# Optimization experiments

Hardware: AMD Instinct MI355X
Metric: run time of the kernel (lower is better)

## Reference

```python
import jax, jax.numpy as jnp
import numpy as np

HEADS = 6
WS = 16          # window_size
OWS = 24         # overlap_win_size
DIM = 192
TABLE = (WS + OWS - 1) ** 2  # 1521


def setup_inputs() -> dict:
    key = jax.random.key(0)
    k1, k2, k3, k4, k5, k6 = jax.random.split(key, 6)
    b = 256
    nq = WS * WS          # 256
    n = OWS * OWS         # 576
    x_q = jax.random.normal(k1, (b, nq, DIM), dtype=jnp.float32)
    x_kv = jax.random.normal(k2, (b, n, DIM), dtype=jnp.float32)
    rpi = jax.random.randint(k3, (nq, n), 0, TABLE, dtype=jnp.int64)
    Wq = jax.random.normal(k4, (DIM, DIM), dtype=jnp.float32) * 0.02
    Wkv = jax.random.normal(k5, (2 * DIM, DIM), dtype=jnp.float32) * 0.02
    bias_table = jax.random.normal(k6, (TABLE, HEADS), dtype=jnp.float32) * 0.02
    return {"x_q": x_q, "x_kv": x_kv, "rpi": rpi, "Wq": Wq, "Wkv": Wkv, "bias_table": bias_table}


def reference(x_q, x_kv, rpi, Wq, Wkv, bias_table):
    b, nq, dim = x_q.shape
    n = x_kv.shape[1]
    hd = dim // HEADS
    scale = hd ** (-0.5)

    # projections (torch Linear: y = x @ W^T)
    q = (x_q @ Wq.T).reshape(b, nq, HEADS, hd).transpose(0, 2, 1, 3)      # b h nq d
    kv = x_kv @ Wkv.T                                                    # b n 2*dim
    k, v = jnp.split(kv, 2, axis=-1)
    k = k.reshape(b, n, HEADS, hd).transpose(0, 2, 1, 3)                  # b h n d
    v = v.reshape(b, n, HEADS, hd).transpose(0, 2, 1, 3)                  # b h n d

    attn = scale * jnp.einsum('bhqd,bhkd->bhqk', q, k)                    # b h nq n

    # gathered relative-position bias: table[rpi] -> (nq, n, h)
    rpb = bias_table[rpi.reshape(-1)].reshape(nq, n, HEADS)
    # nq < n branch in source: permute(2, 0, 1) -> (h, nq, n)
    rpb = rpb.transpose(2, 0, 1)

    attn = jax.nn.softmax(attn + rpb[None], axis=-1)
    out = jnp.einsum('bhqk,bhkd->bhqd', attn, v)                          # b h nq d
    out = out.transpose(0, 2, 1, 3).reshape(b, nq, dim)
    return out
```

## Files before the change

### kernel.cpp

```cpp
#include <hip/hip_runtime.h>
#include <cstdint>

typedef unsigned short u16;
typedef short s16x8 __attribute__((ext_vector_type(8)));
typedef float f32x4 __attribute__((ext_vector_type(4)));
typedef float f32x16 __attribute__((ext_vector_type(16)));

#if __has_builtin(__builtin_amdgcn_exp2f)
#define EXP2(x) __builtin_amdgcn_exp2f(x)
#else
#define EXP2(x) __expf((x)*0.6931471805599453f)
#endif

__device__ __forceinline__ u16 f2bf(float x) {
  uint32_t u = __builtin_bit_cast(uint32_t, x);
  u += 0x7FFFu + ((u >> 16) & 1u);
  return (u16)(u >> 16);
}
__device__ __forceinline__ float bf2f(u16 v) {
  return __builtin_bit_cast(float, (uint32_t)v << 16);
}
__device__ __forceinline__ uint32_t pk_bf16(float lo, float hi) {
  uint32_t ul = __builtin_bit_cast(uint32_t, lo);
  uint32_t uh = __builtin_bit_cast(uint32_t, hi);
  ul += 0x7FFFu + ((ul >> 16) & 1u);
  uh += 0x7FFFu + ((uh >> 16) & 1u);
  return __builtin_amdgcn_perm(uh, ul, 0x07060302u);
}
__device__ __forceinline__ f32x4 mfma16(s16x8 a, s16x8 b, f32x4 c) {
  return __builtin_amdgcn_mfma_f32_16x16x32_bf16(a, b, c, 0, 0, 0);
}
__device__ __forceinline__ f32x16 mfma32(s16x8 a, s16x8 b, f32x16 c) {
  return __builtin_amdgcn_mfma_f32_32x32x16_bf16(a, b, c, 0, 0, 0);
}
__device__ __forceinline__ s16x8 ld_frag(const u16* p) {
  uint4 v = *(const uint4*)p;
  return __builtin_bit_cast(s16x8, v);
}

__global__ void prep_w(const float* __restrict__ Wq, const float* __restrict__ Wkv,
                       u16* __restrict__ wqs, u16* __restrict__ wkvs) {
  int tid = blockIdx.x * 256 + threadIdx.x;
  if (tid >= 13824) return;
  bool isQ = tid < 4608;
  int id = isQ ? tid : tid - 4608;
  int lane = id & 63, fk = id >> 6;
  int kk = fk % 6, fb = fk / 6;
  int f = fb * 16 + (lane & 15), k0 = kk * 32 + ((lane >> 4) << 3);
  const float* src = (isQ ? Wq : Wkv) + (size_t)f * 192 + k0;
  const float sc = isQ ? 0.2550348583f : 1.0f;
  float4 a = ((const float4*)src)[0], b = ((const float4*)src)[1];
  uint4 o;
  o.x = pk_bf16(a.x * sc, a.y * sc); o.y = pk_bf16(a.z * sc, a.w * sc);
  o.z = pk_bf16(b.x * sc, b.y * sc); o.w = pk_bf16(b.z * sc, b.w * sc);
  *(uint4*)&(isQ ? wqs : wkvs)[(size_t)id * 8] = o;
}

__global__ void build_rpb(const int* __restrict__ rpi, const float* __restrict__ table,
                          u16* __restrict__ rpb) {
  const int bi = blockIdx.x;
  const int wv = bi & 7, hk = bi >> 3;
  const int h = hk / 18, kt = hk - h * 18;
  const int lane = threadIdx.x;
  const int u = lane >> 5, l31 = lane & 31;
  const int q = (wv << 5) + l31;
  const int n0 = (kt << 5) + (u << 2);
  u16 vals[16];
#pragma unroll
  for (int g = 0; g < 4; ++g) {
    int4 id4 = *(const int4*)&rpi[q * 576 + n0 + (g << 3)];
    vals[(g << 2) + 0] = f2bf(table[id4.x * 6 + h] * 1.4426950409f);
    vals[(g << 2) + 1] = f2bf(table[id4.y * 6 + h] * 1.4426950409f);
    vals[(g << 2) + 2] = f2bf(table[id4.z * 6 + h] * 1.4426950409f);
    vals[(g << 2) + 3] = f2bf(table[id4.w * 6 + h] * 1.4426950409f);
  }
  uint4* dst = (uint4*)&rpb[((size_t)hk * 512 + (wv << 6) + lane) * 16];
  dst[0] = *(uint4*)&vals[0];
  dst[1] = *(uint4*)&vals[8];
}

template <int G, int MODE>
__device__ __forceinline__ void proj_body(const float* __restrict__ A,
                                          const u16* __restrict__ W,
                                          u16* __restrict__ outQ, u16* __restrict__ outK,
                                          u16* __restrict__ outV, int blk0,
                                          u16* __restrict__ lds) {
  const int t = threadIdx.x, lane = t & 63, w = t >> 6, c = lane & 15, hi = lane >> 4;
  s16x8 wf[G][6];
#pragma unroll
  for (int f = 0; f < G; ++f)
#pragma unroll
    for (int kk = 0; kk < 6; ++kk)
      wf[f][kk] = ld_frag(&W[((size_t)(((w * G + f) * 6 + kk) * 64 + lane)) * 8]);
  const int srow = t >> 4, scol = (t & 15) * 12;
  float4 r0, r1, r2;
  auto ISSUE = [&](int i) {
    const float* src = A + (size_t)((blk0 * 8 + i) * 16 + srow) * 192 + scol;
    r0 = ((const float4*)src)[0];
    r1 = ((const float4*)src)[1];
    r2 = ((const float4*)src)[2];
  };
  auto WRITE = [&](int slot) {
    u16* sl = lds + slot * 3072;
#pragma unroll
    for (int j = 0; j < 3; ++j) {
      float4 v = (j == 0) ? r0 : (j == 1) ? r1 : r2;
      const int c0 = scol + j * 4, kk = c0 >> 5, rem = c0 & 31;
      const int h2 = rem >> 3, e0 = rem & 7;
      uint2 pv;
      pv.x = pk_bf16(v.x, v.y);
      pv.y = pk_bf16(v.z, v.w);
      *(uint2*)&sl[((kk << 6) + (h2 << 4) + srow) * 8 + e0] = pv;
    }
  };
  ISSUE(0); WRITE(0);
  ISSUE(1);
  for (int i = 0; i < 8; ++i) {
    __syncthreads();
    if (i + 1 < 8) WRITE((i + 1) % 3);
    if (i + 2 < 8) ISSUE(i + 2);
    const u16* sl = lds + (i % 3) * 3072;
    s16x8 af[6];
#pragma unroll
    for (int kk = 0; kk < 6; ++kk)
      af[kk] = ld_frag(&sl[((kk << 6) + lane) << 3]);
    f32x4 acc[G];
#pragma unroll
    for (int f = 0; f < G; ++f) acc[f] = f32x4{0.f, 0.f, 0.f, 0.f};
#pragma unroll
    for (int kk = 0; kk < 6; ++kk)
#pragma unroll
      for (int f = 0; f < G; ++f)
        acc[f] = mfma16(wf[f][kk], af[kk], acc[f]);
    const int m = (blk0 * 8 + i) * 16 + c;
#pragma unroll
    for (int f = 0; f < G; ++f) {
      const int fb = ((w * G + f) << 4) + (hi << 2);
      uint2 pv;
      pv.x = pk_bf16(acc[f][0], acc[f][1]);
      pv.y = pk_bf16(acc[f][2], acc[f][3]);
      if (MODE == 0) {
        int b = m >> 8, q = m & 255, hh = fb >> 5, d = fb & 31;
        *(uint2*)&outQ[((((size_t)(b * 6 + hh)) << 8) + q) * 32 + d] = pv;
      } else {
        int b = m / 576, tok = m - b * 576;
        if (fb >= 192) {
          int f2 = fb - 192, hh = f2 >> 5, d = f2 & 31;
          *(uint2*)&outV[(((size_t)(b * 6 + hh)) * 576 + tok) * 32 + d] = pv;
        } else {
          int hh = fb >> 5, dd = fb & 31;
          int half = dd >> 4, uu = (dd >> 3) & 1, e0 = dd & 7;
          int ktt = tok >> 5, lt = tok & 31;
          *(uint2*)&outK[(size_t)((b * 6 + hh) * 18 + ktt) * 1024 +
                         half * 512 + uu * 256 + lt * 8 + e0] = pv;
        }
      }
    }
  }
}

__launch_bounds__(256, 2)
__global__ void proj_all(const float* __restrict__ xq, const float* __restrict__ xkv,
                         const u16* __restrict__ wqs, const u16* __restrict__ wkvs,
                         u16* __restrict__ Qws, u16* __restrict__ Kws,
                         u16* __restrict__ Vws) {
  __shared__ __align__(16) u16 lds[9216];
  int blk = blockIdx.x;
  if (blk < 512) proj_body<3, 0>(xq, wqs, Qws, nullptr, nullptr, blk, lds);
  else           proj_body<6, 1>(xkv, wkvs, nullptr, Kws, Vws, blk - 512, lds);
}

#define VSTR 600
__launch_bounds__(512)
__global__ void attn(const u16* __restrict__ Qws, const u16* __restrict__ Kws,
                     const u16* __restrict__ Vws, const u16* __restrict__ rpb,
                     float* __restrict__ out) {
  __shared__ __align__(16) u16 Vt[32 * VSTR];
  const int bh = blockIdx.x, b = bh / 6, h = bh - b * 6;
  const size_t kvbase = (size_t)bh * 576 * 32;
  const int t = threadIdx.x;
  for (int key = t; key < 576; key += 512) {
    int kk = key & 31, k15 = kk & 15;
    int p = ((kk >> 4) << 4) | (((k15 >> 2) & 1) << 3) | ((k15 >> 3) << 2) | (k15 & 3);
    int col = ((key >> 5) << 5) + p;
    const uint4* src = (const uint4*)&Vws[kvbase + (size_t)key * 32];
    uint4 r[4] = {src[0], src[1], src[2], src[3]};
    const u16* vs = (const u16*)r;
#pragma unroll
    for (int d = 0; d < 32; ++d) Vt[d * VSTR + col] = vs[d];
  }
  const int lane = t & 63, l31 = lane & 31, u = lane >> 5, w = t >> 6;
  const int qg = (w << 5) + l31;
  s16x8 qf[2];
#pragma unroll
  for (int m = 0; m < 2; ++m)
    qf[m] = ld_frag(&Qws[((size_t)bh * 256 + qg) * 32 + (m << 4) + (u << 3)]);
  __syncthreads();
  f32x16 oacc;
#pragma unroll
  for (int r = 0; r < 16; ++r) oacc[r] = 0.f;
  float psum = 0.f;
  const u16* kfb = Kws + (size_t)bh * 18432 + (size_t)lane * 8;
  const u16* bp0 = rpb + (size_t)h * 147456 + (size_t)t * 16;
  s16x8 kA[2], kB[2];
  uint4 bA[2], bB[2];
  kA[0] = ld_frag(kfb);        kB[0] = ld_frag(kfb + 512);
  kA[1] = ld_frag(kfb + 1024); kB[1] = ld_frag(kfb + 1536);
  bA[0] = *(const uint4*)(bp0);        bB[0] = *(const uint4*)(bp0 + 8);
  bA[1] = *(const uint4*)(bp0 + 8192); bB[1] = *(const uint4*)(bp0 + 8192 + 8);
#pragma unroll 2
  for (int kt = 0; kt < 18; ++kt) {
    const int k0 = kt << 5, cur = kt & 1;
    s16x8 vf0 = ld_frag(&Vt[l31 * VSTR + k0 + (u << 3)]);
    s16x8 vf1 = ld_frag(&Vt[l31 * VSTR + k0 + 16 + (u << 3)]);
    f32x16 st;
#pragma unroll
    for (int r = 0; r < 16; ++r) st[r] = 0.f;
    st = mfma32(kA[cur], qf[0], st);
    st = mfma32(kB[cur], qf[1], st);
    uint4 bAc = bA[cur], bBc = bB[cur];
    if (kt < 16) {
      kA[cur] = ld_frag(kfb + (size_t)(kt + 2) * 1024);
      kB[cur] = ld_frag(kfb + (size_t)(kt + 2) * 1024 + 512);
      bA[cur] = *(const uint4*)(bp0 + (size_t)(kt + 2) * 8192);
      bB[cur] = *(const uint4*)(bp0 + (size_t)(kt + 2) * 8192 + 8);
    }
    const u16* b0 = (const u16*)&bAc;
    const u16* b1 = (const u16*)&bBc;
    float e[16];
#pragma unroll
    for (int r = 0; r < 8; ++r)
      e[r] = EXP2(st[r] + bf2f(b0[r]));
#pragma unroll
    for (int r = 8; r < 16; ++r)
      e[r] = EXP2(st[r] + bf2f(b1[r - 8]));
    psum += (((e[0] + e[1]) + (e[2] + e[3])) + ((e[4] + e[5]) + (e[6] + e[7]))) +
            (((e[8] + e[9]) + (e[10] + e[11])) + ((e[12] + e[13]) + (e[14] + e[15])));
    uint4 pa, pb;
    pa.x = pk_bf16(e[0], e[1]);   pa.y = pk_bf16(e[2], e[3]);
    pa.z = pk_bf16(e[4], e[5]);   pa.w = pk_bf16(e[6], e[7]);
    pb.x = pk_bf16(e[8], e[9]);   pb.y = pk_bf16(e[10], e[11]);
    pb.z = pk_bf16(e[12], e[13]); pb.w = pk_bf16(e[14], e[15]);
    s16x8 pf0 = __builtin_bit_cast(s16x8, pa);
    s16x8 pf1 = __builtin_bit_cast(s16x8, pb);
    oacc = mfma32(vf0, pf0, oacc);
    oacc = mfma32(vf1, pf1, oacc);
  }
  float tot = psum + __shfl_xor(psum, 32);
  float rs = 1.0f / tot;
  float* op = out + ((size_t)b * 256 + qg) * 192 + h * 32 + (u << 2);
#pragma unroll
  for (int g = 0; g < 4; ++g) {
    float4 o;
    o.x = oacc[(g << 2) + 0] * rs; o.y = oacc[(g << 2) + 1] * rs;
    o.z = oacc[(g << 2) + 2] * rs; o.w = oacc[(g << 2) + 3] * rs;
    *(float4*)(op + (g << 3)) = o;
  }
}

extern "C" void kernel_launch(void* const* d_in, const int* in_sizes, int n_in,
                              void* d_out, int out_size, void* d_ws, size_t ws_size,
                              hipStream_t stream) {
  const float* x_q   = (const float*)d_in[0];
  const float* x_kv  = (const float*)d_in[1];
  const int*   rpi   = (const int*)d_in[2];
  const float* Wq    = (const float*)d_in[3];
  const float* Wkv   = (const float*)d_in[4];
  const float* table = (const float*)d_in[5];
  float* out = (float*)d_out;

  char* ws = (char*)d_ws;
  u16* wqs  = (u16*)(ws);
  u16* wkvs = (u16*)(ws + 73728);
  u16* rpb  = (u16*)(ws + 221184);
  u16* Qws  = (u16*)(ws + 1990656);
  u16* Kws  = (u16*)(ws + 27156480);
  u16* Vws  = (u16*)(ws + 83779584);

  prep_w<<<54, 256, 0, stream>>>(Wq, Wkv, wqs, wkvs);
  build_rpb<<<864, 64, 0, stream>>>(rpi, table, rpb);
  proj_all<<<1664, 256, 0, stream>>>(x_q, x_kv, wqs, wkvs, Qws, Kws, Vws);
  attn<<<1536, 512, 0, stream>>>(Qws, Kws, Vws, rpb, out);
}
```

Baseline: 337.2 us.

## Load full 128-row tile into LDS upfront instead of triple-buffered pipeline

The projection kernel now has each thread load half a row (24 float4s) of the block's 128-row input tile at once. It converts the values to bf16 into a padded LDS layout (stride 17) to avoid bank conflicts, then runs all 8 MFMA sub-tiles after a single barrier. This removes the per-iteration barriers and the small three-slot software pipeline and issues more memory loads in flight per thread. The cost is more LDS per block (about 52 KB) and many live registers, which may lower occupancy, and no compute now overlaps the loads.

```diff
diff --git a/kernel.cpp b/kernel.cpp
--- a/kernel.cpp
+++ b/kernel.cpp
@@ -79,51 +79,53 @@
   dst[1] = *(uint4*)&vals[8];
 }
 
+#define TPW 17
+#define TILE_U16 (24 * TPW * 8)
 template <int G, int MODE>
 __device__ __forceinline__ void proj_body(const float* __restrict__ A,
                                           const u16* __restrict__ W,
                                           u16* __restrict__ outQ, u16* __restrict__ outK,
-                                          u16* __restrict__ outV, int blk0,
+                                          u16* __restrict__ outV, int blk,
                                           u16* __restrict__ lds) {
   const int t = threadIdx.x, lane = t & 63, w = t >> 6, c = lane & 15, hi = lane >> 4;
+  const int row0 = blk << 7;
+  {
+    const int row = t >> 1, halfc = (t & 1) * 96;
+    const float* src = A + (size_t)(row0 + row) * 192 + halfc;
+    u16* dst = lds + (row >> 4) * TILE_U16;
+    const int srow = row & 15;
+    float4 v[24];
+#pragma unroll
+    for (int j = 0; j < 24; ++j) v[j] = ((const float4*)src)[j];
+#pragma unroll
+    for (int j = 0; j < 24; ++j) {
+      const int c0 = halfc + (j << 2);
+      const int kk = c0 >> 5, h2 = (c0 >> 3) & 3, e0 = c0 & 7;
+      uint2 pv;
+      pv.x = pk_bf16(v[j].x, v[j].y);
+      pv.y = pk_bf16(v[j].z, v[j].w);
+      *(uint2*)&dst[(((kk << 2) + h2) * TPW + srow) * 8 + e0] = pv;
+    }
+  }
   s16x8 wf[G][6];
 #pragma unroll
   for (int f = 0; f < G; ++f)
 #pragma unroll
     for (int kk = 0; kk < 6; ++kk)
       wf[f][kk] = ld_frag(&W[((size_t)(((w * G + f) * 6 + kk) * 64 + lane)) * 8]);
-  const int srow = t >> 4, scol = (t & 15) * 12;
-  float4 r0, r1, r2;
-  auto ISSUE = [&](int i) {
-    const float* src = A + (size_t)((blk0 * 8 + i) * 16 + srow) * 192 + scol;
-    r0 = ((const float4*)src)[0];
-    r1 = ((const float4*)src)[1];
-    r2 = ((const float4*)src)[2];
-  };
-  auto WRITE = [&](int slot) {
-    u16* sl = lds + slot * 3072;
-#pragma unroll
-    for (int j = 0; j < 3; ++j) {
-      float4 v = (j == 0) ? r0 : (j == 1) ? r1 : r2;
-      const int c0 = scol + j * 4, kk = c0 >> 5, rem = c0 & 31;
-      const int h2 = rem >> 3, e0 = rem & 7;
-      uint2 pv;
-      pv.x = pk_bf16(v.x, v.y);
-      pv.y = pk_bf16(v.z, v.w);
-      *(uint2*)&sl[((kk << 6) + (h2 << 4) + srow) * 8 + e0] = pv;
-    }
-  };
-  ISSUE(0); WRITE(0);
-  ISSUE(1);
+#pragma unroll
+  for (int f = 0; f < G; ++f)
+#pragma unroll
+    for (int kk = 0; kk < 6; ++kk)
+      asm volatile("" : "+v"(wf[f][kk]));
+  __syncthreads();
+#pragma unroll
   for (int i = 0; i < 8; ++i) {
-    __syncthreads();
-    if (i + 1 < 8) WRITE((i + 1) % 3);
-    if (i + 2 < 8) ISSUE(i + 2);
-    const u16* sl = lds + (i % 3) * 3072;
+    const u16* sl = lds + i * TILE_U16;
     s16x8 af[6];
 #pragma unroll
     for (int kk = 0; kk < 6; ++kk)
-      af[kk] = ld_frag(&sl[((kk << 6) + lane) << 3]);
+      af[kk] = ld_frag(&sl[(((kk << 2) + hi) * TPW + c) * 8]);
     f32x4 acc[G];
 #pragma unroll
     for (int f = 0; f < G; ++f) acc[f] = f32x4{0.f, 0.f, 0.f, 0.f};
@@ -132,7 +134,7 @@
 #pragma unroll
       for (int f = 0; f < G; ++f)
         acc[f] = mfma16(wf[f][kk], af[kk], acc[f]);
-    const int m = (blk0 * 8 + i) * 16 + c;
+    const int m = row0 + (i << 4) + c;
 #pragma unroll
     for (int f = 0; f < G; ++f) {
       const int fb = ((w * G + f) << 4) + (hi << 2);
@@ -164,7 +166,7 @@
                          const u16* __restrict__ wqs, const u16* __restrict__ wkvs,
                          u16* __restrict__ Qws, u16* __restrict__ Kws,
                          u16* __restrict__ Vws) {
-  __shared__ __align__(16) u16 lds[9216];
+  __shared__ __align__(16) u16 lds[8 * TILE_U16];
   int blk = blockIdx.x;
   if (blk < 512) proj_body<3, 0>(xq, wqs, Qws, nullptr, nullptr, blk, lds);
   else           proj_body<6, 1>(xkv, wkvs, nullptr, Kws, Vws, blk - 512, lds);
```

After: 346.4 us. +2.7%, slower.
